# Performance work log

Hardware: AMD Instinct MI355X
Metric: run time of the kernel (lower is better)

Reference implementation:

```python
import jax, jax.numpy as jnp
import numpy as np

N_EMBD = 1024
N_HEAD = 16
HEAD_DIM = N_EMBD // N_HEAD


def setup_inputs() -> dict:
    key = jax.random.key(0)
    k1, k2, k3 = jax.random.split(key, 3)
    B, T, C = 2, 2048, N_EMBD
    x = jax.random.normal(k1, (B, T, C), dtype=jnp.float32)
    # torch nn.Linear(n_embd, 3*n_embd): weight [3C, C], bias [3C]
    W = jax.random.normal(k2, (3 * C, C), dtype=jnp.float32) * (1.0 / np.sqrt(C))
    b = jax.random.normal(k3, (3 * C,), dtype=jnp.float32) * 0.01
    return {"x": x, "W": W, "b": b}


def reference(x, W, b):
    B, T, C = x.shape
    H, D = N_HEAD, HEAD_DIM
    qkv = jnp.einsum('btc,oc->bto', x, W) + b          # [B,T,3C]
    q, k, v = jnp.split(qkv, 3, axis=2)
    # [B,H,T,D]
    q = q.reshape(B, T, H, D).transpose(0, 2, 1, 3)
    k = k.reshape(B, T, H, D).transpose(0, 2, 1, 3)
    v = v.reshape(B, T, H, D).transpose(0, 2, 1, 3)
    scale = 1.0 / np.sqrt(D).astype(np.float32)
    scores = jnp.einsum('bhid,bhjd->bhij', q, k) * scale   # [B,H,T,T]
    causal = jnp.tril(jnp.ones((T, T), dtype=bool))
    w = jnp.where(causal, jax.nn.relu(scores), 0.0)        # ReLU, no softmax
    y = jnp.einsum('bhij,bhjd->bhid', w, v)                # [B,H,T,D]
    return y.transpose(0, 2, 1, 3).reshape(B, T, C)
```

## Files before the change

### kernel.cpp

```cpp
#include <hip/hip_runtime.h>

typedef __bf16 bf16;
typedef __bf16 bf16x8 __attribute__((ext_vector_type(8)));
typedef float  f32x4  __attribute__((ext_vector_type(4)));

#define T_SEQ   2048
#define D_HEAD  64
#define NH      16
#define BH      32
#define C_EMB   1024
#define WS_STRIDE (BH * T_SEQ * D_HEAD)
#define XN (4096 * 1024)
#define WN (3072 * 1024)
#define WS_NEEDED ((size_t)(3 * WS_STRIDE + XN + WN) * 2)
#define CVT_GRID 3584

__device__ __forceinline__ bf16x8 cvt8(float4 a, float4 b) {
    bf16x8 r;
    r[0] = (__bf16)a.x; r[1] = (__bf16)a.y; r[2] = (__bf16)a.z; r[3] = (__bf16)a.w;
    r[4] = (__bf16)b.x; r[5] = (__bf16)b.y; r[6] = (__bf16)b.z; r[7] = (__bf16)b.w;
    return r;
}

__device__ __forceinline__ void gl_lds16(const bf16* g, bf16* l) {
    __builtin_amdgcn_global_load_lds(
        (const __attribute__((address_space(1))) unsigned int*)g,
        (__attribute__((address_space(3))) unsigned int*)l,
        16, 0, 0);
}

__device__ __forceinline__ unsigned pack_bf16(float a, float b) {
    union { __bf16 h[2]; unsigned u; } pk;
    pk.h[0] = (__bf16)a; pk.h[1] = (__bf16)b;
    return pk.u;
}

__global__ __launch_bounds__(256) void cvt_bf16(
    const float* __restrict__ x, const float* __restrict__ W,
    bf16* __restrict__ xb, bf16* __restrict__ wb)
{
    const int t = blockIdx.x * 256 + threadIdx.x;
    const float* src; bf16* dst; int base;
    if (t < XN / 8) { src = x; dst = xb; base = t * 8; }
    else           { src = W; dst = wb; base = (t - XN / 8) * 8; }
    float4 a = *(const float4*)(src + base);
    float4 b = *(const float4*)(src + base + 4);
    *(bf16x8*)(dst + base) = cvt8(a, b);
}

#define LDA(d, qi) {                                                          \
    const bf16* abase_ = Sh + (d)*16384 + (qi)*8192 + (wm*64 + l15)*64;       \
    _Pragma("unroll")                                                         \
    for (int ii_ = 0; ii_ < 4; ii_++) {                                       \
        _Pragma("unroll")                                                     \
        for (int dk_ = 0; dk_ < 2; dk_++)                                     \
            aF[ii_][dk_] = *(const bf16x8*)(abase_ + ii_*1024                 \
                                            + (((dk_*4 + l4) ^ k7) * 8));     \
    }                                                                         \
}

#define LDB(d, qj, bFv) {                                                     \
    const bf16* bbase_ = Sh + 32768 + (d)*16384 + (qj)*8192                   \
                         + (wn*32 + l15)*64;                                  \
    _Pragma("unroll")                                                         \
    for (int jj_ = 0; jj_ < 2; jj_++) {                                       \
        _Pragma("unroll")                                                     \
        for (int dk_ = 0; dk_ < 2; dk_++)                                     \
            bFv[jj_][dk_] = *(const bf16x8*)(bbase_ + jj_*1024                \
                                             + (((dk_*4 + l4) ^ k7) * 8));    \
    }                                                                         \
}

#define STA(d, qi, s, ko) gl_lds16(                                           \
    aSrc + (size_t)((qi)*64 + (s)*128) * 1024 + (ko),                         \
    Sh + (d)*16384 + (qi)*8192 + (s)*4096 + w*512)

#define STB(d, qj, s, ko) gl_lds16(                                           \
    bSrc + (size_t)((s)*128 + (qj)*32) * 1024 + (ko),                         \
    Sh + 32768 + (d)*16384 + (qj)*8192 + (s)*4096 + w*512)

#define MMAQ(qi, qj, bFv) {                                                   \
    __builtin_amdgcn_s_setprio(1);                                            \
    _Pragma("unroll")                                                         \
    for (int dk_ = 0; dk_ < 2; dk_++) {                                       \
        _Pragma("unroll")                                                     \
        for (int ii_ = 0; ii_ < 4; ii_++) {                                   \
            _Pragma("unroll")                                                 \
            for (int jj_ = 0; jj_ < 2; jj_++)                                 \
                acc[(qi)*4 + ii_][(qj)*2 + jj_] =                             \
                    __builtin_amdgcn_mfma_f32_16x16x32_bf16(                  \
                        aF[ii_][dk_], bFv[jj_][dk_],                          \
                        acc[(qi)*4 + ii_][(qj)*2 + jj_], 0, 0, 0);            \
        }                                                                     \
    }                                                                         \
    __builtin_amdgcn_s_setprio(0);                                            \
}

#define BAR   __builtin_amdgcn_s_barrier()
#define LGKM0 asm volatile("s_waitcnt lgkmcnt(0)" ::: "memory")

#define HALF(d, sk)                                                           \
                                                                      \
    LDA(d, 0) LDB(d, 0, bF0)                                                  \
    BAR; LGKM0;                                                               \
    MMAQ(0, 0, bF0)                                                           \
    BAR;                                                                      \
                                                                      \
    LDB(d, 1, bF1)                                                            \
    STA(d, 0, 0, sk); STA(d, 0, 1, sk); STB(d, 0, 0, sk); STB(d, 0, 1, sk);   \
    BAR; LGKM0;                                                               \
    MMAQ(0, 1, bF1)                                                           \
    BAR;                                                                      \
                                                                      \
    LDA(d, 1)                                                                 \
    STB(d, 1, 0, sk); STB(d, 1, 1, sk);                                       \
    BAR; LGKM0;                                                               \
    MMAQ(1, 0, bF0)                                                           \
    BAR;                                                                      \
                                                                      \
    STA(d, 1, 0, sk); STA(d, 1, 1, sk);                                       \
    BAR;                                                                      \
    MMAQ(1, 1, bF1)                                                           \
    asm volatile("s_waitcnt vmcnt(8)" ::: "memory");                          \
    BAR;

__global__ __launch_bounds__(512, 2) void qkv_gemm3(
    const bf16* __restrict__ xb, const bf16* __restrict__ wb,
    const float* __restrict__ bias, bf16* __restrict__ ws)
{
    __shared__ bf16 Sh[65536];

    const int tid  = threadIdx.x;
    const int lane = tid & 63;
    const int w    = tid >> 6;
    const int wm   = w >> 2, wn = w & 3;
    const int l15  = lane & 15, l4 = lane >> 4;
    const int k7   = l15 & 7;
    const int l8   = lane >> 3;
    const int csw  = (lane & 7) ^ l8;

    const int swz = (blockIdx.x & 7) * 24 + (blockIdx.x >> 3);
    const int bm  = swz / 12, bn = swz % 12;

    const bf16* aSrc = xb + (size_t)(bm * 256 + w * 8 + l8) * 1024 + csw * 8;
    const bf16* bSrc = wb + (size_t)(bn * 256 + (w >> 2) * 64 + (w & 3) * 8 + l8) * 1024
                          + csw * 8;

    f32x4 acc[8][4];
#pragma unroll
    for (int i = 0; i < 8; i++)
#pragma unroll
        for (int j = 0; j < 4; j++) acc[i][j] = (f32x4){0.f, 0.f, 0.f, 0.f};

    bf16x8 aF[4][2], bF0[2][2], bF1[2][2];

    STA(0,0,0,0);  STA(0,0,1,0);  STB(0,0,0,0);  STB(0,0,1,0);
    STB(0,1,0,0);  STB(0,1,1,0);  STA(0,1,0,0);  STA(0,1,1,0);
    STA(1,0,0,64); STA(1,0,1,64); STB(1,0,0,64); STB(1,0,1,64);
    STB(1,1,0,64); STB(1,1,1,64); STA(1,1,0,64); STA(1,1,1,64);
    asm volatile("s_waitcnt vmcnt(8)" ::: "memory");
    BAR;

    for (int it = 0; it < 8; ++it) {
        const int sk0 = (it < 7 ? (2 * it + 2) : 15) * 64;
        const int sk1 = (it < 7 ? (2 * it + 3) : 15) * 64;
        HALF(0, sk0)
        HALF(1, sk1)
    }
    asm volatile("s_waitcnt vmcnt(0)" ::: "memory");
    BAR;

    float bv[4];
#pragma unroll
    for (int j = 0; j < 4; j++) bv[j] = bias[bn * 256 + wn * 64 + j * 16 + l15];

    const int which = bn >> 2;
    const int h     = (bn & 3) * 4 + wn;
    const int bi    = bm >> 3;
    const int tBase = (bm & 7) * 256 + wm * 128;
    const float qs  = (which == 0) ? 0.125f : 1.0f;
    bf16* Wl = Sh + w * 8192;

    if (which < 2) {
#pragma unroll
        for (int i = 0; i < 8; i++)
#pragma unroll
            for (int j = 0; j < 4; j++)
#pragma unroll
                for (int r = 0; r < 4; r++) {
                    const int lm = i * 16 + l4 * 4 + r;
                    const int dd = j * 16 + l15;
                    const int cp = (dd >> 3) ^ (lm & 7);
                    Wl[lm * 64 + cp * 8 + (dd & 7)] =
                        (__bf16)((acc[i][j][r] + bv[j]) * qs);
                }
#pragma unroll
        for (int e = 0; e < 16; e++) {
            const int lm = e * 8 + l8;
            const int c  = lane & 7;
            bf16x8 v8 = *(const bf16x8*)&Wl[lm * 64 + ((c ^ (lm & 7)) * 8)];
            const int t = tBase + lm;
            *(bf16x8*)&ws[(size_t)which * WS_STRIDE
                          + ((size_t)(bi * NH + h) * T_SEQ + t) * D_HEAD + c * 8] = v8;
        }
    } else {
#pragma unroll
        for (int i = 0; i < 8; i++)
#pragma unroll
            for (int j = 0; j < 4; j++) {
                const int dd = j * 16 + l15;
#pragma unroll
                for (int p = 0; p < 2; p++) {
                    const int lm = i * 16 + l4 * 4 + 2 * p;
                    const int ch = lm >> 3;
                    const int cp = (ch & 8) | ((ch & 7) ^ (dd & 7));
                    *(unsigned*)&Wl[dd * 128 + cp * 8 + (lm & 7)] =
                        pack_bf16(acc[i][j][2 * p] + bv[j],
                                  acc[i][j][2 * p + 1] + bv[j]);
                }
            }
        bf16* vt = ws + 2 * (size_t)WS_STRIDE;
#pragma unroll
        for (int e = 0; e < 16; e++) {
            const int dd = e * 4 + l4;
            const int c  = l15;
            const int cp = (c & 8) | ((c & 7) ^ (dd & 7));
            bf16x8 v8 = *(const bf16x8*)&Wl[dd * 128 + cp * 8];
            *(bf16x8*)&vt[((size_t)(bi * NH + h) * D_HEAD + dd) * T_SEQ
                          + tBase + c * 8] = v8;
        }
    }
}

__global__ __launch_bounds__(256) void qkv_gemm(
    const float* __restrict__ x, const float* __restrict__ W,
    const float* __restrict__ bias, bf16* __restrict__ ws)
{
    __shared__ bf16 As[128 * 40];
    __shared__ bf16 Bs[128 * 40];

    const int tid  = threadIdx.x;
    const int lane = tid & 63;
    const int w    = tid >> 6;
    const int wm   = w >> 1, wn = w & 1;
    const int l15  = lane & 15, l4 = lane >> 4;
    const int bm   = blockIdx.x / 24, bn = blockIdx.x % 24;

    const int srow = tid >> 1;
    const int scol = (tid & 1) * 16;
    const float* xg = x + (size_t)(bm * 128 + srow) * 1024 + scol;
    const float* wg = W + (size_t)(bn * 128 + srow) * 1024 + scol;
    bf16* asw = &As[srow * 40 + scol];
    bf16* bsw = &Bs[srow * 40 + scol];

    f32x4 acc[4][4];
#pragma unroll
    for (int i = 0; i < 4; i++)
#pragma unroll
        for (int j = 0; j < 4; j++) acc[i][j] = (f32x4){0.f, 0.f, 0.f, 0.f};

    float bv[4];
#pragma unroll
    for (int j = 0; j < 4; j++) bv[j] = bias[bn * 128 + wn * 64 + j * 16 + l15];

    for (int kk = 0; kk < 32; ++kk) {
        const float* xp = xg + kk * 32;
        const float* wp = wg + kk * 32;
        float4 a0 = *(const float4*)(xp + 0);
        float4 a1 = *(const float4*)(xp + 4);
        float4 a2 = *(const float4*)(xp + 8);
        float4 a3 = *(const float4*)(xp + 12);
        float4 b0 = *(const float4*)(wp + 0);
        float4 b1 = *(const float4*)(wp + 4);
        float4 b2 = *(const float4*)(wp + 8);
        float4 b3 = *(const float4*)(wp + 12);

        __syncthreads();
        *(bf16x8*)(asw + 0) = cvt8(a0, a1);
        *(bf16x8*)(asw + 8) = cvt8(a2, a3);
        *(bf16x8*)(bsw + 0) = cvt8(b0, b1);
        *(bf16x8*)(bsw + 8) = cvt8(b2, b3);
        __syncthreads();

        bf16x8 aF[4], bF[4];
#pragma unroll
        for (int s = 0; s < 4; s++) {
            aF[s] = *(const bf16x8*)&As[(wm * 64 + s * 16 + l15) * 40 + l4 * 8];
            bF[s] = *(const bf16x8*)&Bs[(wn * 64 + s * 16 + l15) * 40 + l4 * 8];
        }
#pragma unroll
        for (int i = 0; i < 4; i++)
#pragma unroll
            for (int j = 0; j < 4; j++)
                acc[i][j] = __builtin_amdgcn_mfma_f32_16x16x32_bf16(
                    aF[i], bF[j], acc[i][j], 0, 0, 0);
    }

#pragma unroll
    for (int i = 0; i < 4; i++) {
#pragma unroll
        for (int j = 0; j < 4; j++) {
            const int n     = bn * 128 + wn * 64 + j * 16 + l15;
            const int which = n >> 10;
            const int cc    = n & 1023;
            const int h     = cc >> 6, d = cc & 63;
            const float qs  = (which == 0) ? 0.125f : 1.0f;
#pragma unroll
            for (int r = 0; r < 4; r++) {
                const int m  = bm * 128 + wm * 64 + i * 16 + l4 * 4 + r;
                const int bi = m >> 11, t = m & 2047;
                const int bh = bi * NH + h;
                const float v = (acc[i][j][r] + bv[j]) * qs;
                size_t idx;
                if (which == 2)
                    idx = 2 * (size_t)WS_STRIDE + ((size_t)bh * D_HEAD + d) * T_SEQ + t;
                else
                    idx = (size_t)which * WS_STRIDE + ((size_t)bh * T_SEQ + t) * D_HEAD + d;
                ws[idx] = (__bf16)v;
            }
        }
    }
}

#define KSTAGE(jt_, p_) {                                                     \
    _Pragma("unroll")                                                         \
    for (int e_ = 0; e_ < 4; e_++) {                                          \
        const int rb_ = w * 32 + e_ * 8;                                      \
        gl_lds16(kg + (size_t)((jt_) * 128 + rb_ + ksub) * 64                 \
                    + ((kc ^ ksub ^ (e_ << 1)) * 8),                          \
                 &Kb[p_][rb_ * 64]);                                          \
    }                                                                         \
}

#define VSTAGE(jt_) {                                                         \
    _Pragma("unroll")                                                         \
    for (int e_ = 0; e_ < 4; e_++) {                                          \
        const int rb_ = w * 16 + e_ * 4;                                      \
        const int sw_ = (rb_ & 12) + vsub;                 \
        gl_lds16(vt + (size_t)(rb_ + vsub) * T_SEQ + (jt_) * 128              \
                    + ((vc ^ sw_) * 8),                                       \
                 &Vts[rb_ * 128]);                                            \
    }                                                                         \
}

__global__ __launch_bounds__(256) void attn(
    const bf16* __restrict__ ws, float* __restrict__ out)
{
    __shared__ bf16 Kb[2][128 * 64];
    __shared__ bf16 Vts[64 * 128];

    const int tid  = threadIdx.x;
    const int lane = tid & 63;
    const int w    = tid >> 6;
    const int l15  = lane & 15, qd = lane >> 4;

    const int bh = blockIdx.x & 31;
    const int u  = blockIdx.x >> 5;
    const int qt = (u < 8) ? u : (23 - u);
    const int nj = qt + 1;
    const int qb = qt * 128;

    const bf16* qg = ws + (size_t)bh * (T_SEQ * D_HEAD);
    const bf16* kg = ws + WS_STRIDE + (size_t)bh * (T_SEQ * D_HEAD);
    const bf16* vt = ws + 2 * (size_t)WS_STRIDE + (size_t)bh * (D_HEAD * T_SEQ);
    const int b = bh >> 4, h = bh & 15;

    const int ksub = lane >> 3;
    const int kc   = lane & 7;
    const int vsub = qd;
    const int vc   = l15;

    const int krow0 = 8 * (l15 >> 2) + (l15 & 3);
    const int pos00 = qd ^ (l15 & 3) ^ ((l15 >> 2) << 1);
    const int kbO0  = krow0 * 64 + pos00 * 8;
    const int kbO1  = krow0 * 64 + (pos00 ^ 4) * 8;

    bf16x8 qF[2][2];
#pragma unroll
    for (int sm = 0; sm < 2; sm++)
#pragma unroll
        for (int dk = 0; dk < 2; dk++)
            qF[sm][dk] = *(const bf16x8*)(qg
                + (qb + w * 32 + sm * 16 + l15) * 64 + dk * 32 + qd * 8);

    f32x4 o[2][4];
#pragma unroll
    for (int sm = 0; sm < 2; sm++)
#pragma unroll
        for (int sd = 0; sd < 4; sd++) o[sm][sd] = (f32x4){0.f, 0.f, 0.f, 0.f};

    KSTAGE(0, 0);

    for (int jt = 0; jt < nj; ++jt) {
        const int p = jt & 1;
        const bool more = (jt + 1 < nj);
        VSTAGE(jt);
        if (more) {
            KSTAGE(jt + 1, p ^ 1);
            asm volatile("s_waitcnt vmcnt(8)" ::: "memory");
        } else {
            asm volatile("s_waitcnt vmcnt(4)" ::: "memory");
        }
        BAR;

        const bf16* kb0 = &Kb[p][kbO0];
        const bf16* kb1 = &Kb[p][kbO1];

        const bool need_mask = (jt == nj - 1);
        unsigned PK[2][8][2];
#pragma unroll
        for (int m = 0; m < 4; m++) {
            bf16x8 kf[2][2];
            kf[0][0] = *(const bf16x8*)(kb0 + m * 2048);
            kf[0][1] = *(const bf16x8*)(kb1 + m * 2048);
            kf[1][0] = *(const bf16x8*)(kb1 + m * 2048 + 256);
            kf[1][1] = *(const bf16x8*)(kb0 + m * 2048 + 256);
#pragma unroll
            for (int h2 = 0; h2 < 2; h2++) {
                const int kn = 2 * m + h2;
                f32x4 s0 = {0.f, 0.f, 0.f, 0.f}, s1 = {0.f, 0.f, 0.f, 0.f};
                __builtin_amdgcn_s_setprio(1);
                s0 = __builtin_amdgcn_mfma_f32_16x16x32_bf16(kf[h2][0], qF[0][0], s0, 0, 0, 0);
                s0 = __builtin_amdgcn_mfma_f32_16x16x32_bf16(kf[h2][1], qF[0][1], s0, 0, 0, 0);
                s1 = __builtin_amdgcn_mfma_f32_16x16x32_bf16(kf[h2][0], qF[1][0], s1, 0, 0, 0);
                s1 = __builtin_amdgcn_mfma_f32_16x16x32_bf16(kf[h2][1], qF[1][1], s1, 0, 0, 0);
                __builtin_amdgcn_s_setprio(0);
                const int keyb = jt * 128 + 32 * m + 8 * qd + 4 * h2;
#pragma unroll
                for (int sm = 0; sm < 2; sm++) {
                    const f32x4 sv = sm ? s1 : s0;
                    float v[4];
#pragma unroll
                    for (int r = 0; r < 4; r++) v[r] = fmaxf(sv[r], 0.f);
                    if (need_mask) {
                        const int q = qb + w * 32 + sm * 16 + l15;
#pragma unroll
                        for (int r = 0; r < 4; r++)
                            if (q < keyb + r) v[r] = 0.f;
                    }
                    PK[sm][kn][0] = pack_bf16(v[0], v[1]);
                    PK[sm][kn][1] = pack_bf16(v[2], v[3]);
                }
            }
        }

        if (more) asm volatile("s_waitcnt vmcnt(4)" ::: "memory");
        else      asm volatile("s_waitcnt vmcnt(0)" ::: "memory");
        BAR;

#pragma unroll
        for (int kk = 0; kk < 4; kk++) {
            bf16x8 pF[2];
#pragma unroll
            for (int sm = 0; sm < 2; sm++) {
                union { unsigned dw[4]; bf16x8 v; } uu;
                uu.dw[0] = PK[sm][2 * kk + 0][0];
                uu.dw[1] = PK[sm][2 * kk + 0][1];
                uu.dw[2] = PK[sm][2 * kk + 1][0];
                uu.dw[3] = PK[sm][2 * kk + 1][1];
                pF[sm] = uu.v;
            }
            __builtin_amdgcn_s_setprio(1);
#pragma unroll
            for (int sd = 0; sd < 4; sd++) {
                bf16x8 vf = *(const bf16x8*)&Vts[(sd * 16 + l15) * 128
                                                 + (((kk * 4 + qd) ^ l15) * 8)];
                o[0][sd] = __builtin_amdgcn_mfma_f32_16x16x32_bf16(pF[0], vf, o[0][sd], 0, 0, 0);
                o[1][sd] = __builtin_amdgcn_mfma_f32_16x16x32_bf16(pF[1], vf, o[1][sd], 0, 0, 0);
            }
            __builtin_amdgcn_s_setprio(0);
        }

        BAR;
    }

#pragma unroll
    for (int sm = 0; sm < 2; sm++)
#pragma unroll
        for (int sd = 0; sd < 4; sd++) {
            const int d = sd * 16 + l15;
#pragma unroll
            for (int r = 0; r < 4; r++) {
                const int t = qb + w * 32 + sm * 16 + qd * 4 + r;
                out[((size_t)b * T_SEQ + t) * C_EMB + h * 64 + d] = o[sm][sd][r];
            }
        }
}

extern "C" void kernel_launch(void* const* d_in, const int* in_sizes, int n_in,
                              void* d_out, int out_size, void* d_ws, size_t ws_size,
                              hipStream_t stream) {
    const float* x    = (const float*)d_in[0];
    const float* W    = (const float*)d_in[1];
    const float* bias = (const float*)d_in[2];
    float* out        = (float*)d_out;
    bf16*  ws         = (bf16*)d_ws;

    if (ws_size >= WS_NEEDED) {
        bf16* xb = ws + 3 * (size_t)WS_STRIDE;
        bf16* wb = xb + XN;
        cvt_bf16<<<dim3(CVT_GRID), dim3(256), 0, stream>>>(x, W, xb, wb);
        qkv_gemm3<<<dim3(192), dim3(512), 0, stream>>>(xb, wb, bias, ws);
    } else {
        qkv_gemm<<<dim3(768), dim3(256), 0, stream>>>(x, W, bias, ws);
    }
    attn<<<dim3(512), dim3(256), 0, stream>>>(ws, out);
}
```

Baseline: 147.2 us.

## Retile QKV GEMM to 256x192 blocks for a 256-block grid

The QKV projection GEMM tile changes from 256x256 to 256x192, so the grid grows from 192 to 256 blocks. That count matches the 256 compute units on MI355X and avoids a partial second wave or idle CUs. The B-operand staging, MFMA schedule (MMA2/MMA1), block swizzle and epilogue are reworked for 48-column warp slices that can straddle head and Q/K/V boundaries in 16-column chunks. In exchange, each block does less reuse of A per B load, and the epilogue gets more complex, with per-chunk branching.

After: 146.9 us. About the same (-0.2%).

```diff
diff --git a/kernel.cpp b/kernel.cpp
--- a/kernel.cpp
+++ b/kernel.cpp
@@ -59,15 +59,14 @@
     }                                                                         \
 }
 
-#define LDB(d, qj, bFv) {                                                     \
-    const bf16* bbase_ = Sh + 32768 + (d)*16384 + (qj)*8192                   \
-                         + (wn*32 + l15)*64;                                  \
+#define LDB(d) {                                                              \
+    const bf16* bbase_ = Sh + 32768 + (d)*12288 + (wn*48 + l15)*64;           \
     _Pragma("unroll")                                                         \
-    for (int jj_ = 0; jj_ < 2; jj_++) {                                       \
+    for (int jj_ = 0; jj_ < 3; jj_++) {                                       \
         _Pragma("unroll")                                                     \
         for (int dk_ = 0; dk_ < 2; dk_++)                                     \
-            bFv[jj_][dk_] = *(const bf16x8*)(bbase_ + jj_*1024                \
-                                             + (((dk_*4 + l4) ^ k7) * 8));    \
+            bF[jj_][dk_] = *(const bf16x8*)(bbase_ + jj_*1024                 \
+                                            + (((dk_*4 + l4) ^ k7) * 8));     \
     }                                                                         \
 }
 
@@ -75,56 +74,65 @@
     aSrc + (size_t)((qi)*64 + (s)*128) * 1024 + (ko),                         \
     Sh + (d)*16384 + (qi)*8192 + (s)*4096 + w*512)
 
-#define STB(d, qj, s, ko) gl_lds16(                                           \
-    bSrc + (size_t)((s)*128 + (qj)*32) * 1024 + (ko),                         \
-    Sh + 32768 + (d)*16384 + (qj)*8192 + (s)*4096 + w*512)
-
-#define MMAQ(qi, qj, bFv) {                                                   \
+#define STB(d, u, ko) gl_lds16(                                               \
+    bSrc + (size_t)((u)*64) * 1024 + (ko),                                    \
+    Sh + 32768 + (d)*12288 + w*512 + (u)*4096)
+
+#define MMA2(qi, ja, jb) {                                                    \
     __builtin_amdgcn_s_setprio(1);                                            \
     _Pragma("unroll")                                                         \
     for (int dk_ = 0; dk_ < 2; dk_++) {                                       \
         _Pragma("unroll")                                                     \
         for (int ii_ = 0; ii_ < 4; ii_++) {                                   \
-            _Pragma("unroll")                                                 \
-            for (int jj_ = 0; jj_ < 2; jj_++)                                 \
-                acc[(qi)*4 + ii_][(qj)*2 + jj_] =                             \
-                    __builtin_amdgcn_mfma_f32_16x16x32_bf16(                  \
-                        aF[ii_][dk_], bFv[jj_][dk_],                          \
-                        acc[(qi)*4 + ii_][(qj)*2 + jj_], 0, 0, 0);            \
+            acc[(qi)*4 + ii_][ja] = __builtin_amdgcn_mfma_f32_16x16x32_bf16(  \
+                aF[ii_][dk_], bF[ja][dk_], acc[(qi)*4 + ii_][ja], 0, 0, 0);   \
+            acc[(qi)*4 + ii_][jb] = __builtin_amdgcn_mfma_f32_16x16x32_bf16(  \
+                aF[ii_][dk_], bF[jb][dk_], acc[(qi)*4 + ii_][jb], 0, 0, 0);   \
         }                                                                     \
     }                                                                         \
     __builtin_amdgcn_s_setprio(0);                                            \
 }
 
+#define MMA1(qi, ja) {                                                        \
+    __builtin_amdgcn_s_setprio(1);                                            \
+    _Pragma("unroll")                                                         \
+    for (int dk_ = 0; dk_ < 2; dk_++) {                                       \
+        _Pragma("unroll")                                                     \
+        for (int ii_ = 0; ii_ < 4; ii_++)                                     \
+            acc[(qi)*4 + ii_][ja] = __builtin_amdgcn_mfma_f32_16x16x32_bf16(  \
+                aF[ii_][dk_], bF[ja][dk_], acc[(qi)*4 + ii_][ja], 0, 0, 0);   \
+    }                                                                         \
+    __builtin_amdgcn_s_setprio(0);                                            \
+}
+
 #define BAR   __builtin_amdgcn_s_barrier()
 #define LGKM0 asm volatile("s_waitcnt lgkmcnt(0)" ::: "memory")
 
 #define HALF(d, sk)                                                           \
                                                                       \
-    LDA(d, 0) LDB(d, 0, bF0)                                                  \
+    LDA(d, 0) LDB(d)                                                          \
     BAR; LGKM0;                                                               \
-    MMAQ(0, 0, bF0)                                                           \
+    MMA2(0, 0, 1)                                                             \
     BAR;                                                                      \
-                                                                      \
-    LDB(d, 1, bF1)                                                            \
-    STA(d, 0, 0, sk); STA(d, 0, 1, sk); STB(d, 0, 0, sk); STB(d, 0, 1, sk);   \
-    BAR; LGKM0;                                                               \
-    MMAQ(0, 1, bF1)                                                           \
+                                                \
+    STB(d, 0, sk); STB(d, 1, sk); STB(d, 2, sk);                              \
+    STA(d, 0, 0, sk); STA(d, 0, 1, sk);                                       \
+    BAR;                                                                      \
+    MMA1(0, 2)                                                                \
     BAR;                                                                      \
                                                                       \
     LDA(d, 1)                                                                 \
-    STB(d, 1, 0, sk); STB(d, 1, 1, sk);                                       \
     BAR; LGKM0;                                                               \
-    MMAQ(1, 0, bF0)                                                           \
+    MMA2(1, 0, 1)                                                             \
     BAR;                                                                      \
-                                                                      \
+                                                    \
     STA(d, 1, 0, sk); STA(d, 1, 1, sk);                                       \
     BAR;                                                                      \
-    MMAQ(1, 1, bF1)                                                           \
-    asm volatile("s_waitcnt vmcnt(8)" ::: "memory");                          \
+    MMA1(1, 2)                                                                \
+    asm volatile("s_waitcnt vmcnt(7)" ::: "memory");                          \
     BAR;
 
-__global__ __launch_bounds__(512, 2) void qkv_gemm3(
+__global__ __launch_bounds__(512, 2) void qkv_gemm4(
     const bf16* __restrict__ xb, const bf16* __restrict__ wb,
     const float* __restrict__ bias, bf16* __restrict__ ws)
 {
@@ -139,26 +147,25 @@
     const int l8   = lane >> 3;
     const int csw  = (lane & 7) ^ l8;
 
-    const int swz = (blockIdx.x & 7) * 24 + (blockIdx.x >> 3);
-    const int bm  = swz / 12, bn = swz % 12;
+    const int swz = (blockIdx.x & 7) * 32 + (blockIdx.x >> 3);
+    const int bm  = swz >> 4, bn = swz & 15;
 
     const bf16* aSrc = xb + (size_t)(bm * 256 + w * 8 + l8) * 1024 + csw * 8;
-    const bf16* bSrc = wb + (size_t)(bn * 256 + (w >> 2) * 64 + (w & 3) * 8 + l8) * 1024
-                          + csw * 8;
-
-    f32x4 acc[8][4];
+    const bf16* bSrc = wb + (size_t)(bn * 192 + w * 8 + l8) * 1024 + csw * 8;
+
+    f32x4 acc[8][3];
 #pragma unroll
     for (int i = 0; i < 8; i++)
 #pragma unroll
-        for (int j = 0; j < 4; j++) acc[i][j] = (f32x4){0.f, 0.f, 0.f, 0.f};
-
-    bf16x8 aF[4][2], bF0[2][2], bF1[2][2];
-
-    STA(0,0,0,0);  STA(0,0,1,0);  STB(0,0,0,0);  STB(0,0,1,0);
-    STB(0,1,0,0);  STB(0,1,1,0);  STA(0,1,0,0);  STA(0,1,1,0);
-    STA(1,0,0,64); STA(1,0,1,64); STB(1,0,0,64); STB(1,0,1,64);
-    STB(1,1,0,64); STB(1,1,1,64); STA(1,1,0,64); STA(1,1,1,64);
-    asm volatile("s_waitcnt vmcnt(8)" ::: "memory");
+        for (int j = 0; j < 3; j++) acc[i][j] = (f32x4){0.f, 0.f, 0.f, 0.f};
+
+    bf16x8 aF[4][2], bF[3][2];
+
+    STA(0,0,0,0);  STA(0,0,1,0);  STA(0,1,0,0);  STA(0,1,1,0);
+    STB(0,0,0);    STB(0,1,0);    STB(0,2,0);
+    STA(1,0,0,64); STA(1,0,1,64); STA(1,1,0,64); STA(1,1,1,64);
+    STB(1,0,64);   STB(1,1,64);   STB(1,2,64);
+    asm volatile("s_waitcnt vmcnt(7)" ::: "memory");
     BAR;
 
     for (int it = 0; it < 8; ++it) {
@@ -170,64 +177,76 @@
     asm volatile("s_waitcnt vmcnt(0)" ::: "memory");
     BAR;
 
-    float bv[4];
-#pragma unroll
-    for (int j = 0; j < 4; j++) bv[j] = bias[bn * 256 + wn * 64 + j * 16 + l15];
-
-    const int which = bn >> 2;
-    const int h     = (bn & 3) * 4 + wn;
+    float bv[3];
+#pragma unroll
+    for (int ff = 0; ff < 3; ff++)
+        bv[ff] = bias[bn * 192 + wn * 48 + ff * 16 + l15];
+
     const int bi    = bm >> 3;
     const int tBase = (bm & 7) * 256 + wm * 128;
-    const float qs  = (which == 0) ? 0.125f : 1.0f;
     bf16* Wl = Sh + w * 8192;
-
-    if (which < 2) {
-#pragma unroll
-        for (int i = 0; i < 8; i++)
-#pragma unroll
-            for (int j = 0; j < 4; j++)
+    bf16* vt = ws + 2 * (size_t)WS_STRIDE;
+
+#pragma unroll
+    for (int ff = 0; ff < 3; ff++) {
+        const int col0 = bn * 192 + wn * 48 + ff * 16;
+        const int wch  = col0 >> 10;
+        const float qs = (wch == 0) ? 0.125f : 1.0f;
+        if (wch < 2) {
+#pragma unroll
+            for (int i = 0; i < 8; i++)
 #pragma unroll
                 for (int r = 0; r < 4; r++) {
-                    const int lm = i * 16 + l4 * 4 + r;
-                    const int dd = j * 16 + l15;
-                    const int cp = (dd >> 3) ^ (lm & 7);
-                    Wl[lm * 64 + cp * 8 + (dd & 7)] =
-                        (__bf16)((acc[i][j][r] + bv[j]) * qs);
+                    const int lt = i * 16 + l4 * 4 + r;
+                    const int dl = l15;
+                    Wl[ff * 2048 + lt * 16 + (((dl >> 3) ^ lt) & 1) * 8 + (dl & 7)]
+                        = (__bf16)((acc[i][ff][r] + bv[ff]) * qs);
                 }
-#pragma unroll
-        for (int e = 0; e < 16; e++) {
-            const int lm = e * 8 + l8;
-            const int c  = lane & 7;
-            bf16x8 v8 = *(const bf16x8*)&Wl[lm * 64 + ((c ^ (lm & 7)) * 8)];
-            const int t = tBase + lm;
-            *(bf16x8*)&ws[(size_t)which * WS_STRIDE
-                          + ((size_t)(bi * NH + h) * T_SEQ + t) * D_HEAD + c * 8] = v8;
-        }
-    } else {
-#pragma unroll
-        for (int i = 0; i < 8; i++)
-#pragma unroll
-            for (int j = 0; j < 4; j++) {
-                const int dd = j * 16 + l15;
+        } else {
+#pragma unroll
+            for (int i = 0; i < 8; i++)
 #pragma unroll
                 for (int p = 0; p < 2; p++) {
-                    const int lm = i * 16 + l4 * 4 + 2 * p;
-                    const int ch = lm >> 3;
-                    const int cp = (ch & 8) | ((ch & 7) ^ (dd & 7));
-                    *(unsigned*)&Wl[dd * 128 + cp * 8 + (lm & 7)] =
-                        pack_bf16(acc[i][j][2 * p] + bv[j],
-                                  acc[i][j][2 * p + 1] + bv[j]);
+                    const int lt0 = i * 16 + l4 * 4 + 2 * p;
+                    const int ct  = lt0 >> 3;
+                    const int dl  = l15;
+                    *(unsigned*)&Wl[ff * 2048 + dl * 128
+                                    + ((ct ^ dl) & 15) * 8 + (lt0 & 7)]
+                        = pack_bf16(acc[i][ff][2 * p] + bv[ff],
+                                    acc[i][ff][2 * p + 1] + bv[ff]);
                 }
-            }
-        bf16* vt = ws + 2 * (size_t)WS_STRIDE;
-#pragma unroll
-        for (int e = 0; e < 16; e++) {
-            const int dd = e * 4 + l4;
-            const int c  = l15;
-            const int cp = (c & 8) | ((c & 7) ^ (dd & 7));
-            bf16x8 v8 = *(const bf16x8*)&Wl[dd * 128 + cp * 8];
-            *(bf16x8*)&vt[((size_t)(bi * NH + h) * D_HEAD + dd) * T_SEQ
-                          + tBase + c * 8] = v8;
+        }
+    }
+    __syncthreads();
+
+#pragma unroll
+    for (int ff = 0; ff < 3; ff++) {
+        const int col0 = bn * 192 + wn * 48 + ff * 16;
+        const int wch  = col0 >> 10;
+        const int cc   = col0 & 1023;
+        const int hh   = cc >> 6;
+        const int dd0  = cc & 63;
+        if (wch < 2) {
+#pragma unroll
+            for (int it = 0; it < 4; it++) {
+                const int lt = it * 32 + (lane >> 1);
+                const int c2 = lane & 1;
+                bf16x8 v8 = *(const bf16x8*)&Wl[ff * 2048 + lt * 16
+                                                + ((c2 ^ lt) & 1) * 8];
+                *(bf16x8*)&ws[(size_t)wch * WS_STRIDE
+                              + ((size_t)(bi * NH + hh) * T_SEQ + tBase + lt) * D_HEAD
+                              + dd0 + c2 * 8] = v8;
+            }
+        } else {
+#pragma unroll
+            for (int e = 0; e < 4; e++) {
+                const int dl = e * 4 + l4;
+                const int ct = l15;
+                bf16x8 v8 = *(const bf16x8*)&Wl[ff * 2048 + dl * 128
+                                                + ((ct ^ dl) & 15) * 8];
+                *(bf16x8*)&vt[((size_t)(bi * NH + hh) * D_HEAD + dd0 + dl) * T_SEQ
+                              + tBase + ct * 8] = v8;
+            }
         }
     }
 }
@@ -500,7 +519,7 @@
         bf16* xb = ws + 3 * (size_t)WS_STRIDE;
         bf16* wb = xb + XN;
         cvt_bf16<<<dim3(CVT_GRID), dim3(256), 0, stream>>>(x, W, xb, wb);
-        qkv_gemm3<<<dim3(192), dim3(512), 0, stream>>>(xb, wb, bias, ws);
+        qkv_gemm4<<<dim3(256), dim3(512), 0, stream>>>(xb, wb, bias, ws);
     } else {
         qkv_gemm<<<dim3(768), dim3(256), 0, stream>>>(x, W, bias, ws);
     }
```
